# Performance work log

Hardware: AMD Instinct MI355X
Metric: run time of the kernel (lower is better)

The kernel has to match this reference:

```python
import jax, jax.numpy as jnp
import numpy as np


def cayley_batch(data):
    # data: (b, r, r). Q = (I + skew) @ (I - skew)^{-1}  (torch solve with left=False)
    b, rr, _ = data.shape
    skew = 0.5 * (data - data.transpose(0, 2, 1))
    I = jnp.eye(rr, dtype=data.dtype)
    A = I - skew  # always invertible (skew-symmetric)
    B = I + skew
    # Solve X @ A = B  ->  A^T X^T = B^T
    Q = jnp.linalg.solve(A.transpose(0, 2, 1), B.transpose(0, 2, 1)).transpose(0, 2, 1)
    return Q


def blockdiag_butterfly_multiply(x, w1, w2):
    # x: (batch, n); w1: (k, q, p) with k*p == n; w2: (l, s, r) with l*r == k*q
    batch = x.shape[0]
    k, q, p = w1.shape
    l, s, r = w2.shape
    out1 = jnp.einsum('bkp,kqp->bkq', x.reshape(batch, k, p), w1)  # (batch, k, q)
    # flat (k*q) viewed as (r, l), then transposed -> (batch, l, r)
    out1 = out1.reshape(batch, r, l).transpose(0, 2, 1)
    out2 = jnp.einsum('blr,lsr->bls', out1, w2)  # (batch, l, s)
    # permute to (batch, s, l) and flatten -> (batch, s*l)
    return out2.transpose(0, 2, 1).reshape(batch, s * l)


def setup_inputs() -> dict:
    key = jax.random.key(0)
    k1, k2, k3 = jax.random.split(key, 3)
    n, nblocks = 4096, 64
    bs = n // nblocks  # 64
    x = jax.random.normal(k1, (16384, n), dtype=jnp.float32)
    L = jax.random.normal(k2, (nblocks, bs, bs), dtype=jnp.float32)
    R = jax.random.normal(k3, (nblocks, bs, bs), dtype=jnp.float32)
    return {"x": x, "L": L, "R": R}


def reference(x, L, R):
    # GSOrthogonal.forward with orthogonal=True, method='cayley':
    # orthogonalize L and R, then butterfly multiply with (x, R_orth, L_orth)
    Lq = cayley_batch(L)
    Rq = cayley_batch(R)
    return blockdiag_butterfly_multiply(x, Rq, Lq)
```

## Files before the change

### kernel.cpp

```cpp
#include <hip/hip_runtime.h>
#include <hip/hip_bf16.h>

typedef __bf16 bf16x4 __attribute__((ext_vector_type(4)));
typedef __bf16 bf16x8 __attribute__((ext_vector_type(8)));
typedef float  floatx4 __attribute__((ext_vector_type(4)));

__global__ __launch_bounds__(256) void cayley_pack_kernel(
    const float* __restrict__ L, const float* __restrict__ R,
    __bf16* __restrict__ ws) {
  __shared__ float Ms[64][65];
  __shared__ float Pa[64];
  __shared__ float Pi[64];
  __shared__ float fcol[2][64];

  const int blk = blockIdx.x;
  const int t = threadIdx.x;
  const float* M = (blk < 64) ? (R + (size_t)blk * 4096)
                              : (L + (size_t)(blk - 64) * 4096);
  __bf16* dst = ws + (size_t)blk * 4096;

  for (int u = 0; u < 16; ++u) {
    int idx = u * 256 + t;
    Ms[idx >> 6][idx & 63] = M[idx];
  }
  __syncthreads();

  const int i = t >> 2;
  const int g = t & 3;
  const int jb = g * 16;
  float a[16], v[16];
#pragma unroll
  for (int jj = 0; jj < 16; ++jj) {
    int j = jb + jj;
    float s = 0.5f * (Ms[i][j] - Ms[j][i]);
    a[jj] = (i == j ? 1.0f : 0.0f) - s;
    v[jj] = (i == j ? 1.0f : 0.0f);
  }
  __syncthreads();

#pragma unroll
  for (int k = 0; k < 64; ++k) {
    if (g == (k >> 4)) fcol[k & 1][i] = a[k & 15];
    __syncthreads();
    if (i == k) {
      float ip = 1.0f / fcol[k & 1][k];
#pragma unroll
      for (int jj = 0; jj < 16; ++jj) {
        a[jj] *= ip; v[jj] *= ip;
        Pa[jb + jj] = a[jj]; Pi[jb + jj] = v[jj];
      }
    }
    __syncthreads();
    if (i != k) {
      float f = fcol[k & 1][i];
#pragma unroll
      for (int jj = 0; jj < 16; ++jj) {
        a[jj] -= f * Pa[jb + jj];
        v[jj] -= f * Pi[jb + jj];
      }
    }
  }

#pragma unroll
  for (int jj = 0; jj < 16; ++jj) {
    int j = jb + jj;
    Ms[i][j] = 2.0f * v[jj] - (i == j ? 1.0f : 0.0f);
  }
  __syncthreads();

  const int lane = t & 63;
  const int grp = t >> 6;
  const int colq = lane & 15;
  const int quad = lane >> 4;
#pragma unroll
  for (int kh = 0; kh < 2; ++kh) {
    bf16x8 pk;
#pragma unroll
    for (int j8 = 0; j8 < 8; ++j8)
      pk[j8] = (__bf16)Ms[16 * grp + colq][32 * kh + 8 * quad + j8];
    *(bf16x8*)(dst + (kh * 4 + grp) * 512 + lane * 8) = pk;
  }
}

__global__ __launch_bounds__(512, 4) void butterfly_kernel(
    const float* __restrict__ x, const __bf16* __restrict__ ws,
    float* __restrict__ out) {
  __shared__ short interS[32768];
  __bf16* inter = (__bf16*)interS;

  const int t = threadIdx.x;
  const int wv = t >> 6;
  const int lane = t & 63;
  const int col = lane & 15;
  const int quad = lane >> 4;
  const size_t b0 = (size_t)blockIdx.x * 8;

  const __bf16* w1 = ws;
  const __bf16* w2 = ws + 64 * 4096;

  const float* xrow = x + (b0 + (size_t)(col & 7)) * 4096;
#pragma unroll
  for (int rg = 0; rg < 2; ++rg) {
    const int r0 = wv * 8 + rg * 4;
    bf16x8 afrag[4][2];
#pragma unroll
    for (int ir = 0; ir < 4; ++ir) {
      const float* src = xrow + (r0 + ir) * 64 + quad * 8;
#pragma unroll
      for (int kh = 0; kh < 2; ++kh) {
        floatx4 u = *(const floatx4*)(src + kh * 32);
        floatx4 w = *(const floatx4*)(src + kh * 32 + 4);
        bf16x8 f;
        f[0] = (__bf16)u[0]; f[1] = (__bf16)u[1];
        f[2] = (__bf16)u[2]; f[3] = (__bf16)u[3];
        f[4] = (__bf16)w[0]; f[5] = (__bf16)w[1];
        f[6] = (__bf16)w[2]; f[7] = (__bf16)w[3];
        afrag[ir][kh] = f;
      }
    }
#pragma unroll
    for (int qc = 0; qc < 4; ++qc) {
      floatx4 vals[4];
#pragma unroll
      for (int ir = 0; ir < 4; ++ir) {
        const int r = r0 + ir;
        bf16x8 bf0 = *(const bf16x8*)(w1 + (size_t)r * 4096 + (0 * 4 + qc) * 512 + lane * 8);
        bf16x8 bf1 = *(const bf16x8*)(w1 + (size_t)r * 4096 + (1 * 4 + qc) * 512 + lane * 8);
        floatx4 acc = {0.f, 0.f, 0.f, 0.f};
        acc = __builtin_amdgcn_mfma_f32_16x16x32_bf16(afrag[ir][0], bf0, acc, 0, 0, 0);
        acc = __builtin_amdgcn_mfma_f32_16x16x32_bf16(afrag[ir][1], bf1, acc, 0, 0, 0);
        vals[ir] = acc;
      }
      if (quad < 2) {
        const int l = qc * 16 + col;
        const int c = r0 >> 3;
        const int ls = l & 7;
#pragma unroll
        for (int reg = 0; reg < 4; ++reg) {
          const int b = quad * 4 + reg;
          bf16x4 pk;
          pk[0] = (__bf16)vals[0][reg];
          pk[1] = (__bf16)vals[1][reg];
          pk[2] = (__bf16)vals[2][reg];
          pk[3] = (__bf16)vals[3][reg];
          const int cs = c ^ b ^ ls;
          *(bf16x4*)(inter + l * 512 + b * 64 + cs * 8 + (r0 & 7)) = pk;
        }
      }
    }
  }
  __syncthreads();

  const int wl = wv & 3;
  const int b = col & 7;
  float* outb = out + b0 * 4096;
#pragma unroll
  for (int sci = 0; sci < 2; ++sci) {
    const int sc = (wv >> 2) * 2 + sci;
    floatx4 vals[16];
#pragma unroll
    for (int l16 = 0; l16 < 16; ++l16) {
      const int l = wl * 16 + l16;
      const int swz = b ^ (l & 7);
      bf16x8 a0 = *(const bf16x8*)(inter + l * 512 + b * 64 + (quad ^ swz) * 8);
      bf16x8 a1 = *(const bf16x8*)(inter + l * 512 + b * 64 + ((4 + quad) ^ swz) * 8);
      bf16x8 bf0 = *(const bf16x8*)(w2 + (size_t)l * 4096 + (0 * 4 + sc) * 512 + lane * 8);
      bf16x8 bf1 = *(const bf16x8*)(w2 + (size_t)l * 4096 + (1 * 4 + sc) * 512 + lane * 8);
      floatx4 acc = {0.f, 0.f, 0.f, 0.f};
      acc = __builtin_amdgcn_mfma_f32_16x16x32_bf16(a0, bf0, acc, 0, 0, 0);
      acc = __builtin_amdgcn_mfma_f32_16x16x32_bf16(a1, bf1, acc, 0, 0, 0);
      vals[l16] = acc;
    }
    if (quad < 2) {
      const int s = sc * 16 + col;
#pragma unroll
      for (int reg = 0; reg < 4; ++reg) {
        const int bb = quad * 4 + reg;
        float* dstp = outb + (size_t)bb * 4096 + s * 64 + wl * 16;
#pragma unroll
        for (int q4 = 0; q4 < 4; ++q4) {
          floatx4 vv;
          vv[0] = vals[q4 * 4 + 0][reg];
          vv[1] = vals[q4 * 4 + 1][reg];
          vv[2] = vals[q4 * 4 + 2][reg];
          vv[3] = vals[q4 * 4 + 3][reg];
          *(floatx4*)(dstp + q4 * 4) = vv;
        }
      }
    }
  }
}

extern "C" void kernel_launch(void* const* d_in, const int* in_sizes, int n_in,
                              void* d_out, int out_size, void* d_ws, size_t ws_size,
                              hipStream_t stream) {
  const float* x = (const float*)d_in[0];
  const float* L = (const float*)d_in[1];
  const float* R = (const float*)d_in[2];
  float* out = (float*)d_out;
  __bf16* ws = (__bf16*)d_ws;

  const int nrows = in_sizes[0] / 4096;

  cayley_pack_kernel<<<128, 256, 0, stream>>>(L, R, ws);
  butterfly_kernel<<<nrows / 8, 512, 0, stream>>>(x, ws, out);
}
```

Measured before the change: 588.7 us.

## Process 16 rows per block to fill MFMA tiles; merge Gauss-Jordan barriers

The butterfly kernel now handles 16 batch rows per block instead of 8. Before, half of each 16-row MFMA tile was padding that got discarded. The intermediate LDS buffer doubles to 128 KB of dynamic shared memory, and occupancy drops to 2 blocks per CU. The Cayley Gauss-Jordan loop double-buffers the pivot row, cutting one barrier per pivot step. The risk is that the 128 KB dynamic LDS request may exceed the default limit and fail to launch if the attribute is not set.

```diff
diff --git a/kernel.cpp b/kernel.cpp
--- a/kernel.cpp
+++ b/kernel.cpp
@@ -9,8 +9,8 @@
     const float* __restrict__ L, const float* __restrict__ R,
     __bf16* __restrict__ ws) {
   __shared__ float Ms[64][65];
-  __shared__ float Pa[64];
-  __shared__ float Pi[64];
+  __shared__ float Pa[2][64];
+  __shared__ float Pi[2][64];
   __shared__ float fcol[2][64];
 
   const int blk = blockIdx.x;
@@ -38,25 +38,25 @@
   }
   __syncthreads();
 
-#pragma unroll
+#pragma unroll 4
   for (int k = 0; k < 64; ++k) {
-    if (g == (k >> 4)) fcol[k & 1][i] = a[k & 15];
+    const int kb = k & 1;
+    if (g == (k >> 4)) fcol[kb][i] = a[k & 15];
+    if (i == k) {
+#pragma unroll
+      for (int jj = 0; jj < 16; ++jj) { Pa[kb][jb + jj] = a[jj]; Pi[kb][jb + jj] = v[jj]; }
+    }
     __syncthreads();
+    const float ip = 1.0f / Pa[kb][k];
     if (i == k) {
-      float ip = 1.0f / fcol[k & 1][k];
+#pragma unroll
+      for (int jj = 0; jj < 16; ++jj) { a[jj] *= ip; v[jj] *= ip; }
+    } else {
+      const float f = fcol[kb][i] * ip;
 #pragma unroll
       for (int jj = 0; jj < 16; ++jj) {
-        a[jj] *= ip; v[jj] *= ip;
-        Pa[jb + jj] = a[jj]; Pi[jb + jj] = v[jj];
-      }
-    }
-    __syncthreads();
-    if (i != k) {
-      float f = fcol[k & 1][i];
-#pragma unroll
-      for (int jj = 0; jj < 16; ++jj) {
-        a[jj] -= f * Pa[jb + jj];
-        v[jj] -= f * Pi[jb + jj];
+        a[jj] -= f * Pa[kb][jb + jj];
+        v[jj] -= f * Pi[kb][jb + jj];
       }
     }
   }
@@ -82,10 +82,10 @@
   }
 }
 
-__global__ __launch_bounds__(512, 4) void butterfly_kernel(
+__global__ __launch_bounds__(512, 2) void butterfly_kernel(
     const float* __restrict__ x, const __bf16* __restrict__ ws,
     float* __restrict__ out) {
-  __shared__ short interS[32768];
+  extern __shared__ short interS[];
   __bf16* inter = (__bf16*)interS;
 
   const int t = threadIdx.x;
@@ -93,12 +93,12 @@
   const int lane = t & 63;
   const int col = lane & 15;
   const int quad = lane >> 4;
-  const size_t b0 = (size_t)blockIdx.x * 8;
+  const size_t b0 = (size_t)blockIdx.x * 16;
 
   const __bf16* w1 = ws;
   const __bf16* w2 = ws + 64 * 4096;
 
-  const float* xrow = x + (b0 + (size_t)(col & 7)) * 4096;
+  const float* xrow = x + (b0 + (size_t)col) * 4096;
 #pragma unroll
   for (int rg = 0; rg < 2; ++rg) {
     const int r0 = wv * 8 + rg * 4;
@@ -131,28 +131,24 @@
         acc = __builtin_amdgcn_mfma_f32_16x16x32_bf16(afrag[ir][1], bf1, acc, 0, 0, 0);
         vals[ir] = acc;
       }
-      if (quad < 2) {
-        const int l = qc * 16 + col;
-        const int c = r0 >> 3;
-        const int ls = l & 7;
-#pragma unroll
-        for (int reg = 0; reg < 4; ++reg) {
-          const int b = quad * 4 + reg;
-          bf16x4 pk;
-          pk[0] = (__bf16)vals[0][reg];
-          pk[1] = (__bf16)vals[1][reg];
-          pk[2] = (__bf16)vals[2][reg];
-          pk[3] = (__bf16)vals[3][reg];
-          const int cs = c ^ b ^ ls;
-          *(bf16x4*)(inter + l * 512 + b * 64 + cs * 8 + (r0 & 7)) = pk;
-        }
+      const int l = qc * 16 + col;
+#pragma unroll
+      for (int reg = 0; reg < 4; ++reg) {
+        const int b = quad * 4 + reg;
+        bf16x4 pk;
+        pk[0] = (__bf16)vals[0][reg];
+        pk[1] = (__bf16)vals[1][reg];
+        pk[2] = (__bf16)vals[2][reg];
+        pk[3] = (__bf16)vals[3][reg];
+        const int cs = wv ^ (b & 7) ^ (l & 7);
+        *(bf16x4*)(inter + l * 1024 + b * 64 + cs * 8 + rg * 4) = pk;
       }
     }
   }
   __syncthreads();
 
   const int wl = wv & 3;
-  const int b = col & 7;
+  const int b = col;
   float* outb = out + b0 * 4096;
 #pragma unroll
   for (int sci = 0; sci < 2; ++sci) {
@@ -161,9 +157,9 @@
 #pragma unroll
     for (int l16 = 0; l16 < 16; ++l16) {
       const int l = wl * 16 + l16;
-      const int swz = b ^ (l & 7);
-      bf16x8 a0 = *(const bf16x8*)(inter + l * 512 + b * 64 + (quad ^ swz) * 8);
-      bf16x8 a1 = *(const bf16x8*)(inter + l * 512 + b * 64 + ((4 + quad) ^ swz) * 8);
+      const int swz = (b & 7) ^ (l & 7);
+      bf16x8 a0 = *(const bf16x8*)(inter + l * 1024 + b * 64 + (quad ^ swz) * 8);
+      bf16x8 a1 = *(const bf16x8*)(inter + l * 1024 + b * 64 + ((4 + quad) ^ swz) * 8);
       bf16x8 bf0 = *(const bf16x8*)(w2 + (size_t)l * 4096 + (0 * 4 + sc) * 512 + lane * 8);
       bf16x8 bf1 = *(const bf16x8*)(w2 + (size_t)l * 4096 + (1 * 4 + sc) * 512 + lane * 8);
       floatx4 acc = {0.f, 0.f, 0.f, 0.f};
@@ -171,21 +167,19 @@
       acc = __builtin_amdgcn_mfma_f32_16x16x32_bf16(a1, bf1, acc, 0, 0, 0);
       vals[l16] = acc;
     }
-    if (quad < 2) {
-      const int s = sc * 16 + col;
-#pragma unroll
-      for (int reg = 0; reg < 4; ++reg) {
-        const int bb = quad * 4 + reg;
-        float* dstp = outb + (size_t)bb * 4096 + s * 64 + wl * 16;
-#pragma unroll
-        for (int q4 = 0; q4 < 4; ++q4) {
-          floatx4 vv;
-          vv[0] = vals[q4 * 4 + 0][reg];
-          vv[1] = vals[q4 * 4 + 1][reg];
-          vv[2] = vals[q4 * 4 + 2][reg];
-          vv[3] = vals[q4 * 4 + 3][reg];
-          *(floatx4*)(dstp + q4 * 4) = vv;
-        }
+    const int s = sc * 16 + col;
+#pragma unroll
+    for (int reg = 0; reg < 4; ++reg) {
+      const int bb = quad * 4 + reg;
+      float* dstp = outb + (size_t)bb * 4096 + s * 64 + wl * 16;
+#pragma unroll
+      for (int q4 = 0; q4 < 4; ++q4) {
+        floatx4 vv;
+        vv[0] = vals[q4 * 4 + 0][reg];
+        vv[1] = vals[q4 * 4 + 1][reg];
+        vv[2] = vals[q4 * 4 + 2][reg];
+        vv[3] = vals[q4 * 4 + 3][reg];
+        *(floatx4*)(dstp + q4 * 4) = vv;
       }
     }
   }
@@ -203,5 +197,5 @@
   const int nrows = in_sizes[0] / 4096;
 
   cayley_pack_kernel<<<128, 256, 0, stream>>>(L, R, ws);
-  butterfly_kernel<<<nrows / 8, 512, 0, stream>>>(x, ws, out);
+  butterfly_kernel<<<nrows / 16, 512, 131072, stream>>>(x, ws, out);
 }
```

Result: slower. 605.5 us (+2.9%).
